# Kernel tuning notes

Hardware: AMD Instinct MI355X
Metric: run time of the kernel (lower is better)

## Reference

```python
import jax, jax.numpy as jnp
import numpy as np

NUM_SEQS = 64
NUM_HEADS = 32
NUM_KV_HEADS = 8
HEAD_DIM = 128
BLOCK_SIZE = 16
MAX_SEQLEN_K = 1024
BLOCKS_PER_SEQ = MAX_SEQLEN_K // BLOCK_SIZE  # 64
NUM_BLOCKS = NUM_SEQS * BLOCKS_PER_SEQ      # 4096
SCALE = 1.0 / float(np.sqrt(HEAD_DIM))
EPS = 1e-6
ROPE_BASE = 10000.0


def setup_inputs() -> dict:
    key = jax.random.key(0)
    ks = jax.random.split(key, 8)
    q = jax.random.normal(ks[0], (NUM_SEQS, NUM_HEADS * HEAD_DIM), jnp.float32)
    k = jax.random.normal(ks[1], (NUM_SEQS, NUM_KV_HEADS * HEAD_DIM), jnp.float32)
    v = jax.random.normal(ks[2], (NUM_SEQS, NUM_KV_HEADS * HEAD_DIM), jnp.float32)
    k_cache = jax.random.normal(ks[3], (NUM_BLOCKS, BLOCK_SIZE, NUM_KV_HEADS, HEAD_DIM), jnp.float32)
    v_cache = jax.random.normal(ks[4], (NUM_BLOCKS, BLOCK_SIZE, NUM_KV_HEADS, HEAD_DIM), jnp.float32)
    qw = 1.0 + 0.1 * jax.random.normal(ks[5], (HEAD_DIM,), jnp.float32)
    kw = 1.0 + 0.1 * jax.random.normal(ks[6], (HEAD_DIM,), jnp.float32)
    # neox rotary cos/sin caches over half the head dim
    inv_freq = 1.0 / (ROPE_BASE ** (jnp.arange(0, HEAD_DIM, 2, dtype=jnp.float32) / HEAD_DIM))
    ang = jnp.arange(MAX_SEQLEN_K, dtype=jnp.float32)[:, None] * inv_freq[None, :]  # [S_max, D/2]
    cos_cache = jnp.cos(ang)
    sin_cache = jnp.sin(ang)
    # decode step: each seq has context_lens tokens already; new token at position context_lens-1
    context_lens = jax.random.randint(ks[7], (NUM_SEQS,), MAX_SEQLEN_K // 2, MAX_SEQLEN_K + 1).astype(jnp.int32)
    position = context_lens - 1
    block_tables = jnp.arange(NUM_SEQS * BLOCKS_PER_SEQ, dtype=jnp.int32).reshape(NUM_SEQS, BLOCKS_PER_SEQ)
    slot_mapping = jnp.arange(NUM_SEQS, dtype=jnp.int32) * MAX_SEQLEN_K + position
    return dict(q=q, k=k, v=v, k_cache=k_cache, v_cache=v_cache, qw=qw, kw=kw,
                cos_cache=cos_cache, sin_cache=sin_cache, position=position,
                slot_mapping=slot_mapping, block_tables=block_tables, context_lens=context_lens)


def _rmsnorm(x, w):
    var = jnp.mean(x * x, axis=-1, keepdims=True)
    return x * jax.lax.rsqrt(var + EPS) * w


def _rope_neox(x, cos, sin):
    # x: [..., D]; cos/sin broadcastable to [..., D/2]
    d = x.shape[-1] // 2
    x1, x2 = x[..., :d], x[..., d:]
    return jnp.concatenate([x1 * cos - x2 * sin, x2 * cos + x1 * sin], axis=-1)


def reference(q, k, v, k_cache, v_cache, qw, kw, cos_cache, sin_cache,
              position, slot_mapping, block_tables, context_lens):
    S = q.shape[0]
    q = q.reshape(S, NUM_HEADS, HEAD_DIM)
    k = k.reshape(S, NUM_KV_HEADS, HEAD_DIM)
    v = v.reshape(S, NUM_KV_HEADS, HEAD_DIM)
    # fused qk-norm + rope
    q = _rmsnorm(q, qw)
    k = _rmsnorm(k, kw)
    cos = cos_cache[position][:, None, :]  # [S,1,D/2]
    sin = sin_cache[position][:, None, :]
    q = _rope_neox(q, cos, sin)
    k = _rope_neox(k, cos, sin)
    # reshape_and_cache: scatter new k/v tokens into the paged cache by flat slot index
    kc = k_cache.reshape(-1, NUM_KV_HEADS, HEAD_DIM).at[slot_mapping].set(k)
    vc = v_cache.reshape(-1, NUM_KV_HEADS, HEAD_DIM).at[slot_mapping].set(v)
    kc = kc.reshape(NUM_BLOCKS, BLOCK_SIZE, NUM_KV_HEADS, HEAD_DIM)
    vc = vc.reshape(NUM_BLOCKS, BLOCK_SIZE, NUM_KV_HEADS, HEAD_DIM)
    # paged attention decode: gather each sequence's blocks
    keys = kc[block_tables].reshape(S, MAX_SEQLEN_K, NUM_KV_HEADS, HEAD_DIM)
    vals = vc[block_tables].reshape(S, MAX_SEQLEN_K, NUM_KV_HEADS, HEAD_DIM)
    G = NUM_HEADS // NUM_KV_HEADS
    qg = q.reshape(S, NUM_KV_HEADS, G, HEAD_DIM)
    scores = jnp.einsum('shgd,snhd->shgn', qg, keys) * SCALE  # [S,KVH,G,N]
    valid = jnp.arange(MAX_SEQLEN_K, dtype=jnp.int32)[None, :] < context_lens[:, None]
    scores = jnp.where(valid[:, None, None, :], scores, -jnp.inf)
    probs = jax.nn.softmax(scores, axis=-1)
    out = jnp.einsum('shgn,snhd->shgd', probs, vals)  # [S,KVH,G,D]
    return out.reshape(S, NUM_HEADS * HEAD_DIM)
```

## Files before the change

### kernel.cpp

```cpp
#include <hip/hip_runtime.h>
#include <math.h>

constexpr int kNumSeqs      = 64;
constexpr int kNumHeads     = 32;
constexpr int kNumKVHeads   = 8;
constexpr int kHeadDim      = 128;
constexpr int kGQA          = 4;
constexpr int kKVBlock      = 16;
constexpr int kMaxSeqlen    = 1024;
constexpr int kBlocksPerSeq = 64;
constexpr int kPart         = 4;
constexpr int kPartSize     = 256;
constexpr float kScale      = 0.08838834764831845f;
constexpr float kEps        = 1e-6f;

constexpr size_t kAccElems = (size_t)kNumSeqs * kNumKVHeads * kPart * kGQA * kHeadDim;
constexpr size_t kMOff     = kAccElems;
constexpr size_t kLOff     = kAccElems + (size_t)kNumSeqs * kNumKVHeads * kPart * kGQA;

__launch_bounds__(256, 4)
__global__ void paged_attn_part(
    const float* __restrict__ q,
    const float* __restrict__ k,
    const float* __restrict__ v,
    const float* __restrict__ k_cache,
    const float* __restrict__ v_cache,
    const float* __restrict__ qw,
    const float* __restrict__ kw,
    const float* __restrict__ cos_cache,
    const float* __restrict__ sin_cache,
    const int*   __restrict__ position,
    const int*   __restrict__ block_tables,
    const int*   __restrict__ context_lens,
    float* __restrict__ ws)
{
  const int bx   = blockIdx.x;
  const int s    = bx >> 5;
  const int h    = (bx >> 2) & 7;
  const int part = bx & 3;
  const int tid  = threadIdx.x;
  const int wave = tid >> 6;
  const int lane = tid & 63;

  const int ctx = context_lens[s];
  const int pos = position[s];
  const int n0  = part * kPartSize;

  float* accw = ws + ((((size_t)s * kNumKVHeads + h) * kPart + part) * kGQA) * kHeadDim;
  float* mw   = ws + kMOff + (((size_t)s * kNumKVHeads + h) * kPart + part) * kGQA;
  float* lw   = ws + kLOff + (((size_t)s * kNumKVHeads + h) * kPart + part) * kGQA;

  if (n0 >= ctx) {
    for (int e = tid; e < kGQA * kHeadDim; e += 256) accw[e] = 0.0f;
    if (tid < kGQA) { mw[tid] = -3.0e38f; lw[tid] = 0.0f; }
    return;
  }
  const int cnt      = min(n0 + kPartSize, ctx) - n0;
  const int posLocal = pos - n0;
  const bool haspos  = (posLocal >= 0) && (posLocal < cnt);

  __shared__ __align__(16) float q_lds[kGQA][kHeadDim];
  __shared__ __align__(16) float kn_lds[kHeadDim];
  __shared__ __align__(16) float vn_lds[kHeadDim];
  __shared__ int bt_lds[kPartSize / kKVBlock];
  __shared__ __align__(16) float macc[8][kGQA][kHeadDim];
  __shared__ float mm[8][kGQA];
  __shared__ float ml[8][kGQA];

  {
    const int g = wave;
    const float* qrow = q + (size_t)s * (kNumHeads * kHeadDim) + (h * kGQA + g) * kHeadDim;
    float x1 = qrow[lane];
    float x2 = qrow[lane + 64];
    float ss = x1 * x1 + x2 * x2;
    for (int off = 32; off >= 1; off >>= 1) ss += __shfl_xor(ss, off);
    const float r = rsqrtf(ss * (1.0f / kHeadDim) + kEps);
    x1 *= r * qw[lane];
    x2 *= r * qw[lane + 64];
    const float c  = cos_cache[pos * 64 + lane];
    const float sn = sin_cache[pos * 64 + lane];
    q_lds[g][lane]      = (x1 * c - x2 * sn) * kScale;
    q_lds[g][lane + 64] = (x2 * c + x1 * sn) * kScale;
  }
  if (wave == 0) {
    const float* krow = k + (size_t)s * (kNumKVHeads * kHeadDim) + h * kHeadDim;
    float x1 = krow[lane];
    float x2 = krow[lane + 64];
    float ss = x1 * x1 + x2 * x2;
    for (int off = 32; off >= 1; off >>= 1) ss += __shfl_xor(ss, off);
    const float r = rsqrtf(ss * (1.0f / kHeadDim) + kEps);
    x1 *= r * kw[lane];
    x2 *= r * kw[lane + 64];
    const float c  = cos_cache[pos * 64 + lane];
    const float sn = sin_cache[pos * 64 + lane];
    kn_lds[lane]      = x1 * c - x2 * sn;
    kn_lds[lane + 64] = x2 * c + x1 * sn;
  } else if (wave == 1) {
    const float* vrow = v + (size_t)s * (kNumKVHeads * kHeadDim) + h * kHeadDim;
    vn_lds[lane]      = vrow[lane];
    vn_lds[lane + 64] = vrow[lane + 64];
  } else if (wave == 2) {
    if (lane < kPartSize / kKVBlock)
      bt_lds[lane] = block_tables[s * kBlocksPerSeq + part * (kPartSize / kKVBlock) + lane];
  }
  __syncthreads();

  const int half = lane >> 5;
  const int l    = lane & 31;

  float4 qf[kGQA];
  #pragma unroll
  for (int g = 0; g < kGQA; ++g)
    qf[g] = *(const float4*)&q_lds[g][4 * l];

  const int npairs = (cnt + 1) >> 1;

  float mrun[kGQA], lrun[kGQA];
  float4 acc[kGQA];
  #pragma unroll
  for (int g = 0; g < kGQA; ++g) {
    mrun[g] = -3.0e38f; lrun[g] = 0.0f;
    acc[g] = make_float4(0.f, 0.f, 0.f, 0.f);
  }

  for (int b = 0; wave + 16 * b < npairs; ++b) {
    float4 kv[4], vv[4];
    bool   val[4];
    #pragma unroll
    for (int jj = 0; jj < 4; ++jj) {
      const int  p  = wave + 16 * b + 4 * jj;
      const bool pv = (p < npairs);
      const int  pp = pv ? p : (npairs - 1);
      const int  n  = 2 * pp + half;
      val[jj] = pv && (n < cnt);
      const int  nn = (n < cnt) ? n : (cnt - 1);
      const int  blk = bt_lds[nn >> 4];
      const size_t base = (((size_t)blk * kKVBlock + (nn & 15)) * kNumKVHeads + h) * kHeadDim;
      kv[jj] = *(const float4*)(k_cache + base + 4 * l);
      vv[jj] = *(const float4*)(v_cache + base + 4 * l);
      if (haspos && nn == posLocal) {
        kv[jj] = *(const float4*)&kn_lds[4 * l];
        vv[jj] = *(const float4*)&vn_lds[4 * l];
      }
    }

    float sg[4][kGQA];
    #pragma unroll
    for (int jj = 0; jj < 4; ++jj) {
      #pragma unroll
      for (int g = 0; g < kGQA; ++g)
        sg[jj][g] = qf[g].x * kv[jj].x + qf[g].y * kv[jj].y +
                    qf[g].z * kv[jj].z + qf[g].w * kv[jj].w;
    }
    #pragma unroll
    for (int off = 16; off >= 1; off >>= 1) {
      #pragma unroll
      for (int jj = 0; jj < 4; ++jj) {
        #pragma unroll
        for (int g = 0; g < kGQA; ++g) sg[jj][g] += __shfl_xor(sg[jj][g], off);
      }
    }
    #pragma unroll
    for (int jj = 0; jj < 4; ++jj) {
      if (!val[jj]) {
        #pragma unroll
        for (int g = 0; g < kGQA; ++g) sg[jj][g] = -3.0e38f;
      }
    }

    #pragma unroll
    for (int g = 0; g < kGQA; ++g) {
      const float mb = fmaxf(fmaxf(sg[0][g], sg[1][g]), fmaxf(sg[2][g], sg[3][g]));
      const float mn = fmaxf(mrun[g], mb);
      const float f  = __expf(mrun[g] - mn);
      const float p0 = __expf(sg[0][g] - mn);
      const float p1 = __expf(sg[1][g] - mn);
      const float p2 = __expf(sg[2][g] - mn);
      const float p3 = __expf(sg[3][g] - mn);
      lrun[g] = lrun[g] * f + (p0 + p1 + p2 + p3);
      acc[g].x = acc[g].x * f + p0 * vv[0].x + p1 * vv[1].x + p2 * vv[2].x + p3 * vv[3].x;
      acc[g].y = acc[g].y * f + p0 * vv[0].y + p1 * vv[1].y + p2 * vv[2].y + p3 * vv[3].y;
      acc[g].z = acc[g].z * f + p0 * vv[0].z + p1 * vv[1].z + p2 * vv[2].z + p3 * vv[3].z;
      acc[g].w = acc[g].w * f + p0 * vv[0].w + p1 * vv[1].w + p2 * vv[2].w + p3 * vv[3].w;
      mrun[g] = mn;
    }
  }

  {
    const int idx = wave * 2 + half;
    #pragma unroll
    for (int g = 0; g < kGQA; ++g)
      *(float4*)&macc[idx][g][4 * l] = acc[g];
    if (l == 0) {
      #pragma unroll
      for (int g = 0; g < kGQA; ++g) { mm[idx][g] = mrun[g]; ml[idx][g] = lrun[g]; }
    }
  }
  __syncthreads();

  for (int e = tid; e < kGQA * kHeadDim; e += 256) {
    const int g = e >> 7;
    const int d = e & 127;
    float ms = mm[0][g];
    #pragma unroll
    for (int i = 1; i < 8; ++i) ms = fmaxf(ms, mm[i][g]);
    float ls = 0.0f, o = 0.0f;
    #pragma unroll
    for (int i = 0; i < 8; ++i) {
      const float w = __expf(mm[i][g] - ms);
      ls += w * ml[i][g];
      o  += w * macc[i][g][d];
    }
    accw[e] = o;
    if (d == 0) { mw[g] = ms; lw[g] = ls; }
  }
}

__launch_bounds__(128)
__global__ void paged_attn_reduce(const float* __restrict__ ws,
                                  float* __restrict__ out)
{
  const int idx = blockIdx.x;
  const int g   = idx & 3;
  const int sh  = idx >> 2;
  const int d   = threadIdx.x;

  const float* mw = ws + kMOff + (size_t)sh * (kPart * kGQA);
  const float* lw = ws + kLOff + (size_t)sh * (kPart * kGQA);

  float m[kPart];
  #pragma unroll
  for (int p = 0; p < kPart; ++p) m[p] = mw[p * kGQA + g];
  float mstar = m[0];
  #pragma unroll
  for (int p = 1; p < kPart; ++p) mstar = fmaxf(mstar, m[p]);

  float w[kPart], lstar = 0.0f;
  #pragma unroll
  for (int p = 0; p < kPart; ++p) {
    w[p] = __expf(m[p] - mstar);
    lstar += w[p] * lw[p * kGQA + g];
  }

  float o = 0.0f;
  #pragma unroll
  for (int p = 0; p < kPart; ++p) {
    const float* accp = ws + (((size_t)sh * kPart + p) * kGQA + g) * kHeadDim;
    o += w[p] * accp[d];
  }
  const int s = sh >> 3, h = sh & 7;
  out[(size_t)s * (kNumHeads * kHeadDim) + (h * kGQA + g) * kHeadDim + d] = o / lstar;
}

extern "C" void kernel_launch(void* const* d_in, const int* in_sizes, int n_in,
                              void* d_out, int out_size, void* d_ws, size_t ws_size,
                              hipStream_t stream) {
  const float* q            = (const float*)d_in[0];
  const float* k            = (const float*)d_in[1];
  const float* v            = (const float*)d_in[2];
  const float* k_cache      = (const float*)d_in[3];
  const float* v_cache      = (const float*)d_in[4];
  const float* qw           = (const float*)d_in[5];
  const float* kw           = (const float*)d_in[6];
  const float* cosc         = (const float*)d_in[7];
  const float* sinc         = (const float*)d_in[8];
  const int*   position     = (const int*)d_in[9];
  const int*   block_tables = (const int*)d_in[11];
  const int*   context_lens = (const int*)d_in[12];
  float* out                = (float*)d_out;
  float* ws                 = (float*)d_ws;

  hipLaunchKernelGGL(paged_attn_part, dim3(kNumSeqs * kNumKVHeads * kPart), dim3(256),
                     0, stream,
                     q, k, v, k_cache, v_cache, qw, kw, cosc, sinc,
                     position, block_tables, context_lens, ws);
  hipLaunchKernelGGL(paged_attn_reduce, dim3(kNumSeqs * kNumKVHeads * kGQA), dim3(kHeadDim),
                     0, stream, ws, out);
}
```

Before: 95.05 us.

## Split KV context into 128-token chunks and skip empty chunks in reduce

```diff
diff --git a/kernel.cpp b/kernel.cpp
--- a/kernel.cpp
+++ b/kernel.cpp
@@ -9,14 +9,15 @@
 constexpr int kKVBlock      = 16;
 constexpr int kMaxSeqlen    = 1024;
 constexpr int kBlocksPerSeq = 64;
-constexpr int kPart         = 4;
-constexpr int kPartSize     = 256;
+constexpr int kChunk        = 128;
+constexpr int kMaxChunks    = kMaxSeqlen / kChunk;
+constexpr int kNumSH        = kNumSeqs * kNumKVHeads;
 constexpr float kScale      = 0.08838834764831845f;
 constexpr float kEps        = 1e-6f;
 
-constexpr size_t kAccElems = (size_t)kNumSeqs * kNumKVHeads * kPart * kGQA * kHeadDim;
+constexpr size_t kAccElems = (size_t)kNumSH * kMaxChunks * kGQA * kHeadDim;
 constexpr size_t kMOff     = kAccElems;
-constexpr size_t kLOff     = kAccElems + (size_t)kNumSeqs * kNumKVHeads * kPart * kGQA;
+constexpr size_t kLOff     = kAccElems + (size_t)kNumSH * kMaxChunks * kGQA;
 
 __launch_bounds__(256, 4)
 __global__ void paged_attn_part(
@@ -34,35 +35,33 @@
     const int*   __restrict__ context_lens,
     float* __restrict__ ws)
 {
-  const int bx   = blockIdx.x;
-  const int s    = bx >> 5;
-  const int h    = (bx >> 2) & 7;
-  const int part = bx & 3;
+  const int item = blockIdx.x;
+  const int c    = item >> 9;
+  const int sh   = item & (kNumSH - 1);
+  const int s    = sh >> 3;
+  const int h    = sh & 7;
+
+  const int ctx = context_lens[s];
+  const int n0  = c * kChunk;
+  if (n0 >= ctx) return;
+
   const int tid  = threadIdx.x;
   const int wave = tid >> 6;
   const int lane = tid & 63;
 
-  const int ctx = context_lens[s];
-  const int pos = position[s];
-  const int n0  = part * kPartSize;
-
-  float* accw = ws + ((((size_t)s * kNumKVHeads + h) * kPart + part) * kGQA) * kHeadDim;
-  float* mw   = ws + kMOff + (((size_t)s * kNumKVHeads + h) * kPart + part) * kGQA;
-  float* lw   = ws + kLOff + (((size_t)s * kNumKVHeads + h) * kPart + part) * kGQA;
-
-  if (n0 >= ctx) {
-    for (int e = tid; e < kGQA * kHeadDim; e += 256) accw[e] = 0.0f;
-    if (tid < kGQA) { mw[tid] = -3.0e38f; lw[tid] = 0.0f; }
-    return;
-  }
-  const int cnt      = min(n0 + kPartSize, ctx) - n0;
+  const int pos      = position[s];
+  const int cnt      = min(n0 + kChunk, ctx) - n0;
   const int posLocal = pos - n0;
   const bool haspos  = (posLocal >= 0) && (posLocal < cnt);
+
+  float* accw = ws + ((size_t)sh * kMaxChunks + c) * kGQA * kHeadDim;
+  float* mw   = ws + kMOff + ((size_t)sh * kMaxChunks + c) * kGQA;
+  float* lw   = ws + kLOff + ((size_t)sh * kMaxChunks + c) * kGQA;
 
   __shared__ __align__(16) float q_lds[kGQA][kHeadDim];
   __shared__ __align__(16) float kn_lds[kHeadDim];
   __shared__ __align__(16) float vn_lds[kHeadDim];
-  __shared__ int bt_lds[kPartSize / kKVBlock];
+  __shared__ int bt_lds[kChunk / kKVBlock];
   __shared__ __align__(16) float macc[8][kGQA][kHeadDim];
   __shared__ float mm[8][kGQA];
   __shared__ float ml[8][kGQA];
@@ -77,10 +76,10 @@
     const float r = rsqrtf(ss * (1.0f / kHeadDim) + kEps);
     x1 *= r * qw[lane];
     x2 *= r * qw[lane + 64];
-    const float c  = cos_cache[pos * 64 + lane];
-    const float sn = sin_cache[pos * 64 + lane];
-    q_lds[g][lane]      = (x1 * c - x2 * sn) * kScale;
-    q_lds[g][lane + 64] = (x2 * c + x1 * sn) * kScale;
+    const float cc  = cos_cache[pos * 64 + lane];
+    const float sn  = sin_cache[pos * 64 + lane];
+    q_lds[g][lane]      = (x1 * cc - x2 * sn) * kScale;
+    q_lds[g][lane + 64] = (x2 * cc + x1 * sn) * kScale;
   }
   if (wave == 0) {
     const float* krow = k + (size_t)s * (kNumKVHeads * kHeadDim) + h * kHeadDim;
@@ -91,17 +90,17 @@
     const float r = rsqrtf(ss * (1.0f / kHeadDim) + kEps);
     x1 *= r * kw[lane];
     x2 *= r * kw[lane + 64];
-    const float c  = cos_cache[pos * 64 + lane];
-    const float sn = sin_cache[pos * 64 + lane];
-    kn_lds[lane]      = x1 * c - x2 * sn;
-    kn_lds[lane + 64] = x2 * c + x1 * sn;
+    const float cc  = cos_cache[pos * 64 + lane];
+    const float sn  = sin_cache[pos * 64 + lane];
+    kn_lds[lane]      = x1 * cc - x2 * sn;
+    kn_lds[lane + 64] = x2 * cc + x1 * sn;
   } else if (wave == 1) {
     const float* vrow = v + (size_t)s * (kNumKVHeads * kHeadDim) + h * kHeadDim;
     vn_lds[lane]      = vrow[lane];
     vn_lds[lane + 64] = vrow[lane + 64];
   } else if (wave == 2) {
-    if (lane < kPartSize / kKVBlock)
-      bt_lds[lane] = block_tables[s * kBlocksPerSeq + part * (kPartSize / kKVBlock) + lane];
+    if (lane < kChunk / kKVBlock)
+      bt_lds[lane] = block_tables[s * kBlocksPerSeq + c * (kChunk / kKVBlock) + lane];
   }
   __syncthreads();
 
@@ -218,37 +217,31 @@
 
 __launch_bounds__(128)
 __global__ void paged_attn_reduce(const float* __restrict__ ws,
+                                  const int* __restrict__ context_lens,
                                   float* __restrict__ out)
 {
   const int idx = blockIdx.x;
   const int g   = idx & 3;
   const int sh  = idx >> 2;
   const int d   = threadIdx.x;
-
-  const float* mw = ws + kMOff + (size_t)sh * (kPart * kGQA);
-  const float* lw = ws + kLOff + (size_t)sh * (kPart * kGQA);
-
-  float m[kPart];
-  #pragma unroll
-  for (int p = 0; p < kPart; ++p) m[p] = mw[p * kGQA + g];
-  float mstar = m[0];
-  #pragma unroll
-  for (int p = 1; p < kPart; ++p) mstar = fmaxf(mstar, m[p]);
-
-  float w[kPart], lstar = 0.0f;
-  #pragma unroll
-  for (int p = 0; p < kPart; ++p) {
-    w[p] = __expf(m[p] - mstar);
-    lstar += w[p] * lw[p * kGQA + g];
-  }
-
-  float o = 0.0f;
-  #pragma unroll
-  for (int p = 0; p < kPart; ++p) {
-    const float* accp = ws + (((size_t)sh * kPart + p) * kGQA + g) * kHeadDim;
-    o += w[p] * accp[d];
-  }
-  const int s = sh >> 3, h = sh & 7;
+  const int s   = sh >> 3;
+  const int h   = sh & 7;
+
+  const int nch = (context_lens[s] + kChunk - 1) / kChunk;
+
+  const float* mw = ws + kMOff + (size_t)sh * (kMaxChunks * kGQA);
+  const float* lw = ws + kLOff + (size_t)sh * (kMaxChunks * kGQA);
+
+  float mstar = -3.0e38f;
+  for (int p = 0; p < nch; ++p) mstar = fmaxf(mstar, mw[p * kGQA + g]);
+
+  float lstar = 0.0f, o = 0.0f;
+  for (int p = 0; p < nch; ++p) {
+    const float w = __expf(mw[p * kGQA + g] - mstar);
+    lstar += w * lw[p * kGQA + g];
+    const float* accp = ws + ((size_t)sh * kMaxChunks + p) * kGQA * kHeadDim + (size_t)g * kHeadDim;
+    o += w * accp[d];
+  }
   out[(size_t)s * (kNumHeads * kHeadDim) + (h * kGQA + g) * kHeadDim + d] = o / lstar;
 }
 
@@ -270,10 +263,9 @@
   float* out                = (float*)d_out;
   float* ws                 = (float*)d_ws;
 
-  hipLaunchKernelGGL(paged_attn_part, dim3(kNumSeqs * kNumKVHeads * kPart), dim3(256),
-                     0, stream,
+  hipLaunchKernelGGL(paged_attn_part, dim3(kMaxChunks * kNumSH), dim3(256), 0, stream,
                      q, k, v, k_cache, v_cache, qw, kw, cosc, sinc,
                      position, block_tables, context_lens, ws);
-  hipLaunchKernelGGL(paged_attn_reduce, dim3(kNumSeqs * kNumKVHeads * kGQA), dim3(kHeadDim),
-                     0, stream, ws, out);
+  hipLaunchKernelGGL(paged_attn_reduce, dim3(kNumSH * kGQA), dim3(kHeadDim), 0, stream,
+                     ws, context_lens, out);
 }
```

Result: no change. 94.41 us (-0.7%).
